# Optimization experiments

Hardware: AMD Instinct MI355X
Metric: run time of the kernel (lower is better)

Reference implementation:

```python
import jax, jax.numpy as jnp
import numpy as np
import itertools, math

CUTOFF = 10.0
ON_CUT = 0.25 * CUTOFF
OFF_CUT = 0.75 * CUTOFF
ALPHA = 4.0 / CUTOFF + 0.001
ALPHA2 = ALPHA ** 2
TWO_PI = 2.0 * math.pi
ONE_OVER_SQRTPI = 1.0 / math.sqrt(math.pi)
B = 512      # molecules
NA = 128     # atoms per molecule
N = B * NA   # total atoms
DEG = 64     # neighbors per atom
P = N * DEG  # total pairs


def _make_kvecs(Nmax=(2, 2, 2)):
    ks = []
    for i in range(3):
        kk = list(range(Nmax[i] + 1)) + [-v for v in range(1, Nmax[i] + 1)]
        ks.append(kk)
    lk = list(itertools.product(*ks))[1:]  # drop (0,0,0)
    kv = np.array(lk, dtype=np.float32)
    kmax = max(Nmax)
    return jnp.asarray(kv[(kv ** 2).sum(-1) <= kmax ** 2])  # [32,3]


def setup_inputs() -> dict:
    key = jax.random.key(0)
    k1, k2, k3, k4, k5, k6 = jax.random.split(key, 6)
    Z = jax.random.randint(k1, (N,), 1, 94)
    Qa = 0.2 * jax.random.normal(k2, (N,), dtype=jnp.float32)
    R = 20.0 * jax.random.uniform(k3, (N, 3), dtype=jnp.float32)
    Dij = 0.5 + 9.5 * jax.random.uniform(k4, (P,), dtype=jnp.float32)
    idx_i = jnp.repeat(jnp.arange(N), DEG)
    idx_j = (idx_i // NA) * NA + jax.random.randint(k5, (P,), 0, NA)
    batch_seg = jnp.repeat(jnp.arange(B), NA)
    Cell = jnp.tile(20.0 * jnp.eye(3, dtype=jnp.float32), (B, 1, 1)) \
           + 0.05 * jax.random.normal(k6, (B, 3, 3), dtype=jnp.float32)
    kvecs = _make_kvecs()
    return dict(Dij=Dij, Qa=Qa, R=R, Cell=Cell, kvecs=kvecs,
                Z=Z, idx_i=idx_i, idx_j=idx_j, batch_seg=batch_seg)


def _switch_function(x):
    # infinitely smooth switch from 1 (x<=on) to 0 (x>=off)
    def comp(t):
        t_ = jnp.where(t <= 0, 1.0, t)
        return jnp.where(t <= 0, 0.0, jnp.exp(-1.0 / t_))
    x = (x - ON_CUT) / (OFF_CUT - ON_CUT)
    fp = comp(x)
    fm = comp(1.0 - x)
    return jnp.where(x <= 0, 1.0, jnp.where(x >= 1, 0.0, fm / (fp + fm)))


def reference(Dij, Qa, R, Cell, kvecs, Z, idx_i, idx_j, batch_seg):
    # ---- real space: gather -> elementwise -> segment_sum ----
    fac = Qa[idx_i] * Qa[idx_j]                              # [P]
    f = _switch_function(Dij)
    coulomb = 1.0 / Dij
    damped = 1.0 / jnp.sqrt(Dij * Dij + 1.0)
    pw = fac * (f * damped + (1.0 - f) * coulomb) * jax.lax.erfc(ALPHA * Dij)
    e_real = 0.5 * jax.ops.segment_sum(pw, idx_i, num_segments=N)  # [N]

    # ---- reciprocal space ----
    recip_box = TWO_PI * jnp.transpose(jnp.linalg.inv(Cell), (0, 2, 1))  # [B,3,3]
    v_box = jnp.abs(jnp.linalg.det(Cell))                    # [B]
    prefactor = TWO_PI / v_box                               # [B]
    k = jnp.einsum('kx,bxy->bky', kvecs, recip_box)          # [B,K,3]
    k2 = jnp.sum(k * k, axis=-1)                             # [B,K]
    qg = jnp.exp(-0.25 * k2 / ALPHA2)                        # [B,K]
    kd = jnp.einsum('nkx,nx->nk', k[batch_seg], R)           # [N,K]
    q_real = jax.ops.segment_sum(Qa[:, None] * jnp.cos(kd), batch_seg, num_segments=B)  # [B,K]
    q_imag = jax.ops.segment_sum(Qa[:, None] * jnp.sin(kd), batch_seg, num_segments=B)  # [B,K]
    q_dens = q_real ** 2 + q_imag ** 2
    # NOTE: faithful to TF source: reduce over ALL axes -> scalar, then * prefactor [B]
    e_reciprocal = prefactor * jnp.sum(q_dens * qg / k2)     # [B]
    e_self = -ALPHA * ONE_OVER_SQRTPI * jax.ops.segment_sum(Qa * Qa, batch_seg, num_segments=B)
    QaR = jax.ops.segment_sum(Qa[:, None] * R, batch_seg, num_segments=B)  # [B,3]
    e_bc = prefactor / 3.0 * jnp.sum(QaR * QaR, axis=-1)     # [B]
    e_rec_tot = e_reciprocal + e_self + e_bc                 # [B]

    Na_per_batch = jax.ops.segment_sum(jnp.ones_like(batch_seg, dtype=Qa.dtype),
                                       batch_seg, num_segments=B)
    er = (e_rec_tot / Na_per_batch)[batch_seg]               # per-atom broadcast [N]
    return e_real + er, Qa
```

## Files before the change

kernel.cpp:

```cpp
#include <hip/hip_runtime.h>
#include <math.h>

#define ON_CUT_C   2.5f
#define OFF_CUT_C  7.5f
#define ALPHA_C    0.401f
#define ALPHA2_C   0.160801f
#define TWO_PI_C   6.2831853071795864f
#define INV_SQRT_PI_C 0.56418958354775628f
#define NB   512
#define NA_C 128
#define NTOT (NB*NA_C)
#define DEG_C 64
#define KC   32
#define NPTS 4096
#define TSCALE (4096.0f / 9.5f)

#define RCP(x) __builtin_amdgcn_rcpf(x)
#define RSQ(x) __builtin_amdgcn_rsqf(x)

__device__ __forceinline__ float fast_erfc(float x) {
    float t = RCP(1.0f + 0.3275911f * x);
    float p = t*(0.254829592f + t*(-0.284496736f +
              t*(1.421413741f + t*(-1.453152027f + t*1.061405429f))));
    return p * __expf(-x*x);
}

__device__ __forceinline__ float pair_g(float D) {
    float x  = (D - ON_CUT_C) * (1.0f / (OFF_CUT_C - ON_CUT_C));
    float xc = fminf(fmaxf(x, 1e-12f), 0.99999994f);
    float gg = RCP(1.0f - xc) - RCP(xc);
    float f  = RCP(1.0f + __expf(gg));
    float coulomb = RCP(D);
    float damped  = RSQ(D*D + 1.0f);
    return (f*damped + (1.0f - f)*coulomb) * fast_erfc(ALPHA_C * D);
}

__global__ __launch_bounds__(512, 4) void ewald_fused_kernel(
    const float* __restrict__ Dij, const float* __restrict__ Qa,
    const float* __restrict__ R, const float* __restrict__ Cell,
    const float* __restrict__ kvecs, const int* __restrict__ idx_j,
    float* __restrict__ ws, float* __restrict__ out)
{
    int b   = blockIdx.x;
    int tid = threadIdx.x;

    __shared__ float4 sar[NA_C];
    __shared__ float  sqa[NA_C];
    __shared__ float skx[KC], sky[KC], skz[KC], sgok2[KC];
    __shared__ float pr[KC][17], pi[KC][17];
    __shared__ float redw[2][4];
    __shared__ float s_pref;
    __shared__ float tabv[NPTS + 1];

    if (tid < NA_C) {
        int n = b * NA_C + tid;
        float qa = Qa[n];
        sar[tid] = make_float4(qa, R[n*3+0], R[n*3+1], R[n*3+2]);
        sqa[tid] = qa;
    }
    for (int i = tid; i <= NPTS; i += 512) {
        float D0 = 0.5f + (9.5f / (float)NPTS) * (float)i;
        tabv[i] = pair_g(D0);
    }
    if (tid < KC) {
        const float* C = Cell + b * 9;
        float c00=C[0], c01=C[1], c02=C[2];
        float c10=C[3], c11=C[4], c12=C[5];
        float c20=C[6], c21=C[7], c22=C[8];
        float m00 = c11*c22 - c12*c21;
        float m01 = c02*c21 - c01*c22;
        float m02 = c01*c12 - c02*c11;
        float m10 = c12*c20 - c10*c22;
        float m11 = c00*c22 - c02*c20;
        float m12 = c02*c10 - c00*c12;
        float m20 = c10*c21 - c11*c20;
        float m21 = c01*c20 - c00*c21;
        float m22 = c00*c11 - c01*c10;
        float det = c00*m00 + c01*m10 + c02*m20;
        float invdet = 1.0f / det;
        float kv0 = kvecs[tid*3+0], kv1 = kvecs[tid*3+1], kv2 = kvecs[tid*3+2];
        float kx = TWO_PI_C * invdet * (m00*kv0 + m01*kv1 + m02*kv2);
        float ky = TWO_PI_C * invdet * (m10*kv0 + m11*kv1 + m12*kv2);
        float kz = TWO_PI_C * invdet * (m20*kv0 + m21*kv1 + m22*kv2);
        float k2 = kx*kx + ky*ky + kz*kz;
        skx[tid] = kx; sky[tid] = ky; skz[tid] = kz;
        sgok2[tid] = __expf(-0.25f * k2 / ALPHA2_C) / k2;
        if (tid == 0) s_pref = TWO_PI_C / fabsf(det);
    }
    __syncthreads();

    int atom_l = tid >> 2;
    int il     = tid & 3;
    const float* Dp = Dij   + ((size_t)(b * NA_C + atom_l) * DEG_C + il * 4);
    const int*   Jp = idx_j + ((size_t)(b * NA_C + atom_l) * DEG_C + il * 4);
    float4 D4[4]; int4 J4[4];
    #pragma unroll
    for (int c = 0; c < 4; ++c) {
        D4[c] = *(const float4*)(Dp + c * 16);
        J4[c] = *(const int4*)(Jp + c * 16);
    }

    {
        int k = tid & 31, chunk = tid >> 5;
        float kx = skx[k], ky = sky[k], kz = skz[k];
        float cr = 0.0f, ci = 0.0f;
        int a0 = chunk * 8;
        #pragma unroll
        for (int i = 0; i < 8; ++i) {
            float4 ar = sar[a0 + i];
            float kd = kx*ar.y + ky*ar.z + kz*ar.w;
            cr += ar.x * __cosf(kd);
            ci += ar.x * __sinf(kd);
        }
        pr[k][chunk] = cr; pi[k][chunk] = ci;
    }

    if (tid < NA_C) {
        float4 ar = sar[tid];
        float q2 = ar.x*ar.x, px = ar.x*ar.y, py = ar.x*ar.z, pz = ar.x*ar.w;
        #pragma unroll
        for (int off = 32; off; off >>= 1) {
            q2 += __shfl_down(q2, off, 64);
            px += __shfl_down(px, off, 64);
            py += __shfl_down(py, off, 64);
            pz += __shfl_down(pz, off, 64);
        }
        if ((tid & 63) == 0) {
            int w = tid >> 6;
            redw[w][0]=q2; redw[w][1]=px; redw[w][2]=py; redw[w][3]=pz;
        }
    }

    float qi = sqa[atom_l];
    float pw = 0.0f;
    #pragma unroll
    for (int c = 0; c < 4; ++c) {
        float Dv[4] = {D4[c].x, D4[c].y, D4[c].z, D4[c].w};
        int   jv[4] = {J4[c].x, J4[c].y, J4[c].z, J4[c].w};
        #pragma unroll
        for (int e = 0; e < 4; ++e) {
            float qj = sqa[jv[e] & (NA_C - 1)];
            int   i  = (int)fmaf(Dv[e] - 0.5f, TSCALE, 0.5f);
            pw += (qi * qj) * tabv[i];
        }
    }
    pw += __shfl_xor(pw, 1, 64);
    pw += __shfl_xor(pw, 2, 64);
    if (il == 0) out[b * NA_C + atom_l] = 0.5f * pw;

    __syncthreads();
    if (tid < KC) {
        float r = 0.0f, im = 0.0f;
        #pragma unroll
        for (int c = 0; c < 16; ++c) { r += pr[tid][c]; im += pi[tid][c]; }
        float sterm = (r*r + im*im) * sgok2[tid];
        #pragma unroll
        for (int off = 16; off; off >>= 1) sterm += __shfl_down(sterm, off, 64);
        if (tid == 0) {
            ws[b] = sterm;
            float q2t = redw[0][0] + redw[1][0];
            float X  = redw[0][1] + redw[1][1];
            float Y  = redw[0][2] + redw[1][2];
            float Zc = redw[0][3] + redw[1][3];
            ws[NB + b] = s_pref;
            ws[2*NB + b] = -ALPHA_C * INV_SQRT_PI_C * q2t
                           + (s_pref * (1.0f/3.0f)) * (X*X + Y*Y + Zc*Zc);
        }
    }
}

__global__ __launch_bounds__(128) void finalize_kernel(
    const float* __restrict__ ws, const float* __restrict__ Qa,
    float* __restrict__ out)
{
    int b   = blockIdx.x;
    int tid = threadIdx.x;
    __shared__ float s_er;

    int n = b * NA_C + tid;
    out[NTOT + n] = Qa[n];

    if (tid < 64) {
        float s = 0.0f;
        #pragma unroll
        for (int i = 0; i < 8; ++i) s += ws[tid + 64*i];
        #pragma unroll
        for (int off = 32; off; off >>= 1) s += __shfl_xor(s, off, 64);
        if (tid == 0)
            s_er = (ws[NB + b] * s + ws[2*NB + b]) * (1.0f / NA_C);
    }
    __syncthreads();

    out[n] += s_er;
}

extern "C" void kernel_launch(void* const* d_in, const int* in_sizes, int n_in,
                              void* d_out, int out_size, void* d_ws, size_t ws_size,
                              hipStream_t stream) {
    const float* Dij   = (const float*)d_in[0];
    const float* Qa    = (const float*)d_in[1];
    const float* R     = (const float*)d_in[2];
    const float* Cell  = (const float*)d_in[3];
    const float* kvecs = (const float*)d_in[4];
    const int*   idx_j = (const int*)d_in[7];
    float* ws  = (float*)d_ws;
    float* out = (float*)d_out;

    ewald_fused_kernel<<<NB, 512, 0, stream>>>(Dij, Qa, R, Cell, kvecs, idx_j, ws, out);
    finalize_kernel<<<NB, NA_C, 0, stream>>>(ws, Qa, out);
}
```

Baseline: 14.74 us.

## Shrink pair lookup table with linear interpolation and replicate LDS arrays

Cuts the per-block pair-function table from 4097 to 513 entries and switches from nearest-point lookup to linear interpolation. This reduces the pair_g evaluations (exp, rcp, erfc) each block performs in its prologue. It also replicates the charge array four times with rotated offsets and the table twice, so that different lane groups hit different LDS banks during the random gathers. The cost is an extra table read and a few more ALU ops per pair, plus a small change in accuracy.

```diff
diff --git a/kernel.cpp b/kernel.cpp
--- a/kernel.cpp
+++ b/kernel.cpp
@@ -12,8 +12,9 @@
 #define NTOT (NB*NA_C)
 #define DEG_C 64
 #define KC   32
-#define NPTS 4096
-#define TSCALE (4096.0f / 9.5f)
+#define NPTS 512
+#define TSCALE (512.0f / 9.5f)
+#define TREP  520
 
 #define RCP(x) __builtin_amdgcn_rcpf(x)
 #define RSQ(x) __builtin_amdgcn_rsqf(x)
@@ -45,22 +46,26 @@
     int tid = threadIdx.x;
 
     __shared__ float4 sar[NA_C];
-    __shared__ float  sqa[NA_C];
+    __shared__ float  sqa_rep[4 * NA_C];
     __shared__ float skx[KC], sky[KC], skz[KC], sgok2[KC];
     __shared__ float pr[KC][17], pi[KC][17];
     __shared__ float redw[2][4];
     __shared__ float s_pref;
-    __shared__ float tabv[NPTS + 1];
+    __shared__ float tabr[2 * TREP];
 
     if (tid < NA_C) {
         int n = b * NA_C + tid;
         float qa = Qa[n];
         sar[tid] = make_float4(qa, R[n*3+0], R[n*3+1], R[n*3+2]);
-        sqa[tid] = qa;
+        #pragma unroll
+        for (int r = 0; r < 4; ++r)
+            sqa_rep[r * NA_C + ((tid + 8*r) & (NA_C - 1))] = qa;
     }
     for (int i = tid; i <= NPTS; i += 512) {
         float D0 = 0.5f + (9.5f / (float)NPTS) * (float)i;
-        tabv[i] = pair_g(D0);
+        float v  = pair_g(D0);
+        tabr[i] = v;
+        tabr[TREP + i] = v;
     }
     if (tid < KC) {
         const float* C = Cell + b * 9;
@@ -131,7 +136,12 @@
         }
     }
 
-    float qi = sqa[atom_l];
+    int lane   = tid & 63;
+    int grp4   = lane >> 4;
+    int sqoff  = grp4 * NA_C;
+    int sqrot  = 8 * grp4;
+    int tboff  = ((lane >> 5) & 1) * TREP;
+    float qi = sqa_rep[atom_l & (NA_C - 1)];
     float pw = 0.0f;
     #pragma unroll
     for (int c = 0; c < 4; ++c) {
@@ -139,9 +149,14 @@
         int   jv[4] = {J4[c].x, J4[c].y, J4[c].z, J4[c].w};
         #pragma unroll
         for (int e = 0; e < 4; ++e) {
-            float qj = sqa[jv[e] & (NA_C - 1)];
-            int   i  = (int)fmaf(Dv[e] - 0.5f, TSCALE, 0.5f);
-            pw += (qi * qj) * tabv[i];
+            float qj  = sqa_rep[sqoff + (((jv[e] & (NA_C-1)) + sqrot) & (NA_C-1))];
+            float idx = fminf((Dv[e] - 0.5f) * TSCALE, 511.9995f);
+            float fi  = floorf(idx);
+            float u   = idx - fi;
+            int   i   = tboff + (int)fi;
+            float v0  = tabr[i];
+            float v1  = tabr[i + 1];
+            pw += (qi * qj) * fmaf(v1 - v0, u, v0);
         }
     }
     pw += __shfl_xor(pw, 1, 64);
```

Result: no change. 14.68 us (-0.4%).
